# Optimization experiments

Measured on AMD Instinct MI355X. Metric: run time of the kernel, lower is better.

The kernel has to match this reference:

```python
import jax, jax.numpy as jnp
import numpy as np

# dims: B nodes, K hops, N neighbors/node, channels/features per FeatTrans1d stage
B, K, N = 512, 2, 32
C0, F0 = 1, 512
C1, F1 = 4, 16
C2, F2 = 32, 1
NUM_CLASS = 40
EPS_BN = 1e-5
EPS_NORM = 1e-7


def softsign(x):
    return x / (1.0 + jnp.abs(x))


def sgnroot(x):
    return jnp.sign(x) * jnp.sqrt(jnp.abs(x))


def row_normalize(x):
    # normalize over axis 1 as in the torch code; NaN -> 0
    x = x / (jnp.abs(x).sum(axis=1, keepdims=True) + EPS_NORM)
    return jnp.where(jnp.isnan(x), 0.0, x)


def feature_adjacency(x, nb):
    # x: [B,C,F], nb: [B,N,C,F] -> fadj: [B,F,F]
    fadj = jnp.einsum('bcf,bncg->bfg', x, nb)
    fadj = fadj + jnp.swapaxes(fadj, -1, -2)
    return row_normalize(sgnroot(fadj))


def transform(x, fadj, W):
    # x: [B,C,F], fadj: [B,F,G], W: [D,C,G,E] -> [B,D,E]
    xg = jnp.einsum('bcf,bfg->bcg', x, fadj)
    return jnp.einsum('bcg,dcge->bde', xg, W)


def transform_nb(nb, fadj, W):
    # nb: [B,N,C,F], fadj: [B,F,G] (node i's fadj broadcast over its N neighbors)
    xg = jnp.einsum('bncf,bfg->bncg', nb, fadj)
    return jnp.einsum('bncg,dcge->bnde', xg, W)


def bn(x, gamma, beta, axes, ch_axis):
    # training-mode BatchNorm1d: batch stats per channel (biased variance)
    mean = x.mean(axes, keepdims=True)
    var = x.var(axes, keepdims=True)
    shape = [1] * x.ndim
    shape[ch_axis] = x.shape[ch_axis]
    return (x - mean) * jax.lax.rsqrt(var + EPS_BN) * gamma.reshape(shape) + beta.reshape(shape)


def setup_inputs() -> dict:
    key = jax.random.key(0)
    ks = jax.random.split(key, 8)
    x = jax.random.normal(ks[0], (B, C0, F0), jnp.float32)
    neighbor = jax.random.normal(ks[1], (B, K, N, C0, F0), jnp.float32)
    W1 = jax.random.normal(ks[2], (K, C1, C0, F0, F1), jnp.float32) * 0.05
    W2 = jax.random.normal(ks[3], (K, C2, C1, F1, F2), jnp.float32) * 0.1
    g1 = jnp.ones((K, C1), jnp.float32)
    b1 = jnp.zeros((K, C1), jnp.float32)
    g2 = jnp.ones((K, C2), jnp.float32)
    b2 = jnp.zeros((K, C2), jnp.float32)
    Wc1 = jax.random.normal(ks[4], (C2 * F2 * K, C2 * F2), jnp.float32) * 0.1
    bc1 = jnp.zeros((C2 * F2,), jnp.float32)
    Wc2 = jax.random.normal(ks[5], (C2 * F2, NUM_CLASS), jnp.float32) * 0.1
    bc2 = jnp.zeros((NUM_CLASS,), jnp.float32)
    return {"x": x, "neighbor": neighbor, "W1": W1, "g1": g1, "b1": b1,
            "W2": W2, "g2": g2, "b2": b2,
            "Wc1": Wc1, "bc1": bc1, "Wc2": Wc2, "bc2": bc2}


def reference(x, neighbor, W1, g1, b1, W2, g2, b2, Wc1, bc1, Wc2, bc2):
    outs = []
    for kk in range(K):  # fixed small hop count, structurally distinct weights
        nb_k = neighbor[:, kk]                      # [B,N,C0,F0]
        fadj1 = feature_adjacency(x, nb_k)          # [B,F0,F0]
        h = transform(x, fadj1, W1[kk])             # [B,C1,F1]
        nbh = transform_nb(nb_k, fadj1, W1[kk])     # [B,N,C1,F1]
        # BN over batch+feature dims for h; per-node BN over (N,F) for neighbors
        h = softsign(bn(h, g1[kk], b1[kk], (0, 2), 1))
        nbh = softsign(bn(nbh, g1[kk], b1[kk], (1, 3), 2))
        fadj2 = feature_adjacency(h, nbh)           # [B,F1,F1]
        h2 = transform(h, fadj2, W2[kk])            # [B,C2,F2]
        h2 = softsign(bn(h2, g2[kk], b2[kk], (0, 2), 1))
        outs.append(h2)
    x_khops = jnp.concatenate(outs, axis=1)         # [B, C2*K, F2]
    flat = x_khops.reshape(B, -1)                   # dropout is identity at eval
    hid = jax.nn.relu(flat @ Wc1 + bc1)
    return hid @ Wc2 + bc2                          # [B, NUM_CLASS]
```

## Files before the change

kernel.cpp:

```cpp
#include <hip/hip_runtime.h>
#include <hip/hip_bf16.h>

#define B_SZ 512
#define KHOP 2
#define NNB  32
#define F0   512
#define C1   4
#define F1   16
#define C2   32
#define NCLS 40

#define EPS_BN   1e-5f
#define EPS_NORM 1e-7f

typedef __attribute__((ext_vector_type(8))) short short8;
typedef __attribute__((ext_vector_type(4))) float f32x4;

__device__ __forceinline__ float softsignf(float v) { return v / (1.0f + fabsf(v)); }

__device__ __forceinline__ unsigned cvt_pk_bf16(float lo, float hi) {
    unsigned r;
    asm("v_cvt_pk_bf16_f32 %0, %1, %2" : "=v"(r) : "v"(lo), "v"(hi));
    return r;
}

__global__ __launch_bounds__(256) void k_prep(const float* __restrict__ W1,
                                              unsigned short* __restrict__ w1t)
{
    const int idx = blockIdx.x * 256 + threadIdx.x;
    const int g  = idx & 511;
    const int de = (idx >> 9) & 63;
    const int kk = idx >> 15;
    const int d = de >> 4, e = de & 15;
    w1t[idx] = (unsigned short)cvt_pk_bf16(W1[((size_t)((kk * 4 + d) * 512) + g) * 16 + e], 0.f);
}

#define SMEM_MAIN 69632

__global__ __launch_bounds__(512, 4) void k_main(
    const float* __restrict__ xg_, const float* __restrict__ nbg,
    const unsigned short* __restrict__ w1t,
    const float* __restrict__ g1, const float* __restrict__ b1,
    float* __restrict__ h_raw, float* __restrict__ nbs_out,
    float* __restrict__ hsum)
{
    extern __shared__ char smem[];
    float* xl = (float*)(smem + 65536);
    float* sl = (float*)(smem + 67584);

    const int t = threadIdx.x;
    const int pair = blockIdx.x;
    const int b = pair >> 1, k = pair & 1;
    const int l = t & 63, w = t >> 6;
    const int m = w & 1, gsb = w >> 1;
    const int kol = l >> 4;
    const float* nbp = nbg + (size_t)pair * (NNB * F0);

    {
        const int oct = t & 63, ng = t >> 6;
        const int f0s = oct * 8;
        float sp0=0,sp1=0,sp2=0,sp3=0,sp4=0,sp5=0,sp6=0,sp7=0;
        #pragma unroll
        for (int ni = 0; ni < 4; ++ni) {
            const int n = ng * 4 + ni;
            float4 q0 = *(const float4*)(nbp + n * F0 + f0s);
            float4 q1 = *(const float4*)(nbp + n * F0 + f0s + 4);
            sp0 += q0.x; sp1 += q0.y; sp2 += q0.z; sp3 += q0.w;
            sp4 += q1.x; sp5 += q1.y; sp6 += q1.z; sp7 += q1.w;
            uint4 p;
            p.x = cvt_pk_bf16(q0.x, q0.y);
            p.y = cvt_pk_bf16(q0.z, q0.w);
            p.z = cvt_pk_bf16(q1.x, q1.y);
            p.w = cvt_pk_bf16(q1.z, q1.w);
            *(uint4*)(smem + n * 1024 + ((2 * f0s) ^ ((n & 7) << 4))) = p;
        }
        float* part = (float*)(smem + 32768);
        *(float4*)(part + ng * 512 + f0s)     = make_float4(sp0, sp1, sp2, sp3);
        *(float4*)(part + ng * 512 + f0s + 4) = make_float4(sp4, sp5, sp6, sp7);
        xl[t] = xg_[b * F0 + t];
    }
    __syncthreads();
    {
        const float* part = (const float*)(smem + 32768);
        float s = 0.f;
        #pragma unroll
        for (int p = 0; p < 8; ++p) s += part[p * 512 + t];
        sl[t] = s;
    }
    __syncthreads();

    const float xv = xl[t], sv = sl[t];
    float dS0 = 0.f, dS1 = 0.f, xS0 = 0.f, xS1 = 0.f;
    f32x4 acc[8];
    #pragma unroll
    for (int j = 0; j < 8; ++j) acc[j] = (f32x4){0.f, 0.f, 0.f, 0.f};

    const int swz = ((t >> 1) & 3) << 4;
    const int nA  = m * 16 + (l & 15);
    const int aSw = (nA & 7) << 4;

    #pragma unroll 1
    for (int strip = 0; strip < 16; ++strip) {
        const int f0 = strip * 32;
        #pragma unroll
        for (int ko = 0; ko < 4; ++ko) {
            float4 xf0 = ((const float4*)xl)[(f0 >> 2) + ko * 2];
            float4 xf1 = ((const float4*)xl)[(f0 >> 2) + ko * 2 + 1];
            float4 sf0 = ((const float4*)sl)[(f0 >> 2) + ko * 2];
            float4 sf1 = ((const float4*)sl)[(f0 >> 2) + ko * 2 + 1];
            const float xf[8] = {xf0.x, xf0.y, xf0.z, xf0.w, xf1.x, xf1.y, xf1.z, xf1.w};
            const float sf[8] = {sf0.x, sf0.y, sf0.z, sf0.w, sf1.x, sf1.y, sf1.z, sf1.w};
            unsigned pk[4];
            float vprev = 0.f;
            #pragma unroll
            for (int i = 0; i < 8; ++i) {
                float r = sf[i] * xv + xf[i] * sv;
                float a = sqrtf(fabsf(r));
                float v = copysignf(a, r);
                if (i & 1) {
                    dS1 += a; xS1 += xf[i] * v;
                    pk[i >> 1] = cvt_pk_bf16(vprev, v);
                } else {
                    dS0 += a; xS0 += xf[i] * v;
                    vprev = v;
                }
            }
            uint4 u; u.x = pk[0]; u.y = pk[1]; u.z = pk[2]; u.w = pk[3];
            *(uint4*)(smem + 32768 + t * 64 + ((ko * 16) ^ swz)) = u;
        }
        __syncthreads();
        short8 afrag = *(const short8*)(smem + nA * 1024 +
                        ((f0 * 2 + kol * 16) ^ aSw));
        #pragma unroll
        for (int j = 0; j < 8; ++j) {
            const int g = gsb * 128 + j * 16 + (l & 15);
            short8 bfrag = *(const short8*)(smem + 32768 + g * 64 +
                            ((kol * 16) ^ (((g >> 1) & 3) << 4)));
            acc[j] = __builtin_amdgcn_mfma_f32_16x16x32_bf16(afrag, bfrag, acc[j], 0, 0, 0);
        }
        __syncthreads();
    }

    {
        const float ia = 1.f / ((dS0 + dS1) + EPS_NORM);
        ((float*)(smem + 32768))[t] = ia;
        ((float*)(smem + 34816))[t] = (xS0 + xS1) * ia;
    }
    __syncthreads();

    {
        const float* invD = (const float*)(smem + 32768);
        #pragma unroll
        for (int j = 0; j < 8; ++j) {
            const int g = gsb * 128 + j * 16 + (l & 15);
            const float iv = invD[g];
            #pragma unroll
            for (int r = 0; r < 4; ++r) {
                const int n = m * 16 + (l >> 4) * 4 + r;
                *(unsigned short*)(smem + n * 1024 + ((2 * g) ^ ((n & 7) << 4))) =
                    (unsigned short)cvt_pk_bf16(acc[j][r] * iv, 0.f);
            }
        }
    }
    __syncthreads();

    f32x4 acc3 = (f32x4){0.f, 0.f, 0.f, 0.f};
    f32x4 acch = (f32x4){0.f, 0.f, 0.f, 0.f};
    {
        const int de = gsb * 16 + (l & 15);
        const unsigned short* wtp = w1t + ((size_t)(k * 64 + de) * 512) + kol * 8;
        const float* xgx = (const float*)(smem + 34816);
        #pragma unroll 2
        for (int ks = 0; ks < 16; ++ks) {
            short8 bfrag = *(const short8*)(wtp + ks * 32);
            short8 af = *(const short8*)(smem + nA * 1024 +
                        ((ks * 64 + kol * 16) ^ aSw));
            acc3 = __builtin_amdgcn_mfma_f32_16x16x32_bf16(af, bfrag, acc3, 0, 0, 0);
            if (m == 0) {
                short8 afh = {0, 0, 0, 0, 0, 0, 0, 0};
                if ((l & 15) == 0) {
                    float4 p0 = *(const float4*)(xgx + ks * 32 + kol * 8);
                    float4 p1 = *(const float4*)(xgx + ks * 32 + kol * 8 + 4);
                    uint4 pk;
                    pk.x = cvt_pk_bf16(p0.x, p0.y); pk.y = cvt_pk_bf16(p0.z, p0.w);
                    pk.z = cvt_pk_bf16(p1.x, p1.y); pk.w = cvt_pk_bf16(p1.z, p1.w);
                    __builtin_memcpy(&afh, &pk, 16);
                }
                acch = __builtin_amdgcn_mfma_f32_16x16x32_bf16(afh, bfrag, acch, 0, 0, 0);
            }
        }
    }

    float* redst = (float*)(smem + 32768);
    float* pnb   = (float*)(smem + 32832);
    {
        float vals[4];
        float s1 = 0.f, s2 = 0.f;
        #pragma unroll
        for (int r = 0; r < 4; ++r) {
            float v = acc3[r];
            vals[r] = v; s1 += v; s2 += v * v;
        }
        #pragma unroll
        for (int off = 32; off >= 1; off >>= 1) {
            s1 += __shfl_xor(s1, off);
            s2 += __shfl_xor(s2, off);
        }
        if (l == 0) { redst[w * 2] = s1; redst[w * 2 + 1] = s2; }
        __syncthreads();
        const float S1 = redst[w * 2]     + redst[(w ^ 1) * 2];
        const float S2 = redst[w * 2 + 1] + redst[(w ^ 1) * 2 + 1];
        const float mean = S1 * (1.f / 512.f);
        const float var  = S2 * (1.f / 512.f) - mean * mean;
        const float An   = g1[k * C1 + gsb] * rsqrtf(var + EPS_BN);
        const float Bn   = b1[k * C1 + gsb] - mean * An;
        float nbse = 0.f;
        #pragma unroll
        for (int r = 0; r < 4; ++r) nbse += softsignf(vals[r] * An + Bn);
        nbse += __shfl_xor(nbse, 16);
        nbse += __shfl_xor(nbse, 32);
        if (l < 16) pnb[m * 64 + gsb * 16 + l] = nbse;

        if (m == 0 && l < 16) {
            float hv = acch[0];
            h_raw[pair * 64 + gsb * 16 + l] = hv;
            float t1 = hv, t2 = hv * hv;
            #pragma unroll
            for (int off = 1; off <= 8; off <<= 1) {
                t1 += __shfl_xor(t1, off);
                t2 += __shfl_xor(t2, off);
            }
            if (l == 0) {
                atomicAdd(&hsum[k * 4 + gsb], t1);
                atomicAdd(&hsum[8 + k * 4 + gsb], t2);
            }
        }
    }
    __syncthreads();
    if (t < 64) nbs_out[pair * 64 + t] = pnb[t] + pnb[64 + t];
}

__global__ __launch_bounds__(256) void k_stage2(
    const float* __restrict__ h_rawg, const float* __restrict__ nbsg,
    const float* __restrict__ hsum,
    const float* __restrict__ g1, const float* __restrict__ b1,
    const float* __restrict__ W2,
    float* __restrict__ h2_raw, float* __restrict__ h2sum)
{
    __shared__ float hl[4][64], nl[4][64], fl[4][256], xg2l[4][64];
    const int t = threadIdx.x, wv = t >> 6, l = t & 63;
    const int pair = blockIdx.x * 4 + wv;
    const int k = pair & 1;
    const int d = l >> 4;
    {
        const float S1 = hsum[k * 4 + d], S2 = hsum[8 + k * 4 + d];
        const float mean = S1 * (1.f / 8192.f);
        const float var  = S2 * (1.f / 8192.f) - mean * mean;
        const float A = g1[k * 4 + d] * rsqrtf(var + EPS_BN);
        const float Bc = b1[k * 4 + d] - mean * A;
        float hv = h_rawg[pair * 64 + l];
        hl[wv][l] = softsignf(hv * A + Bc);
        nl[wv][l] = nbsg[pair * 64 + l];
    }
    __syncthreads();
    const int gcol = l & 15;
    float raw[4];
    #pragma unroll
    for (int j = 0; j < 4; ++j) {
        const int idx = l + 64 * j;
        const int f = idx >> 4;
        float a = 0.f;
        #pragma unroll
        for (int c = 0; c < 4; ++c) a += hl[wv][c * 16 + f] * nl[wv][c * 16 + gcol];
        raw[j] = a;
        fl[wv][idx] = a;
    }
    __syncthreads();
    float w4[4]; float Dp = 0.f;
    #pragma unroll
    for (int j = 0; j < 4; ++j) {
        const int idx = l + 64 * j;
        const int f = idx >> 4;
        float v = raw[j] + fl[wv][gcol * 16 + f];
        float a = sqrtf(fabsf(v));
        Dp += a;
        w4[j] = copysignf(a, v);
    }
    Dp += __shfl_xor(Dp, 16);
    Dp += __shfl_xor(Dp, 32);
    const float invD = 1.f / (Dp + EPS_NORM);
    __syncthreads();
    #pragma unroll
    for (int j = 0; j < 4; ++j) fl[wv][l + 64 * j] = w4[j] * invD;
    __syncthreads();
    {
        const int c = l >> 4;
        float a = 0.f;
        #pragma unroll
        for (int f = 0; f < 16; ++f) a += hl[wv][c * 16 + f] * fl[wv][f * 16 + gcol];
        xg2l[wv][c * 16 + gcol] = a;
    }
    __syncthreads();
    if (l < 32) {
        const float* W2p = W2 + k * (C2 * C1 * F1) + l * (C1 * F1);
        float a = 0.f;
        #pragma unroll
        for (int i = 0; i < 64; ++i) a += xg2l[wv][i] * W2p[i];
        h2_raw[pair * 32 + l] = a;
        atomicAdd(&h2sum[k * 32 + l], a);
        atomicAdd(&h2sum[64 + k * 32 + l], a * a);
    }
}

__global__ __launch_bounds__(64) void k_cls(
    const float* __restrict__ h2_raw, const float* __restrict__ h2sum,
    const float* __restrict__ g2, const float* __restrict__ b2,
    const float* __restrict__ Wc1, const float* __restrict__ bc1,
    const float* __restrict__ Wc2, const float* __restrict__ bc2,
    float* __restrict__ out)
{
    __shared__ float flat[64];
    __shared__ float hid[32];
    const int b = blockIdx.x, l = threadIdx.x;
    const int k = l >> 5, d = l & 31;
    {
        const float S1 = h2sum[l], S2 = h2sum[64 + l];
        const float mean = S1 * (1.f / 512.f);
        const float var  = S2 * (1.f / 512.f) - mean * mean;
        const float A = g2[l] * rsqrtf(var + EPS_BN);
        const float Bc = b2[l] - mean * A;
        float v = h2_raw[(b * 2 + k) * 32 + d];
        flat[l] = softsignf(v * A + Bc);
    }
    __syncthreads();
    if (l < 32) {
        float a = bc1[l];
        #pragma unroll
        for (int i = 0; i < 64; ++i) a += flat[i] * Wc1[i * 32 + l];
        hid[l] = fmaxf(a, 0.f);
    }
    __syncthreads();
    if (l < NCLS) {
        float a = bc2[l];
        #pragma unroll
        for (int j = 0; j < 32; ++j) a += hid[j] * Wc2[j * NCLS + l];
        out[b * NCLS + l] = a;
    }
}

extern "C" void kernel_launch(void* const* d_in, const int* in_sizes, int n_in,
                              void* d_out, int out_size, void* d_ws, size_t ws_size,
                              hipStream_t stream)
{
    const float* x   = (const float*)d_in[0];
    const float* nbg = (const float*)d_in[1];
    const float* W1  = (const float*)d_in[2];
    const float* g1  = (const float*)d_in[3];
    const float* b1  = (const float*)d_in[4];
    const float* W2  = (const float*)d_in[5];
    const float* g2  = (const float*)d_in[6];
    const float* b2  = (const float*)d_in[7];
    const float* Wc1 = (const float*)d_in[8];
    const float* bc1 = (const float*)d_in[9];
    const float* Wc2 = (const float*)d_in[10];
    const float* bc2 = (const float*)d_in[11];
    float* out = (float*)d_out;
    float* ws  = (float*)d_ws;

    float* h_raw  = ws;
    float* nbs    = ws + 65536;
    float* h2_raw = ws + 131072;
    float* stats  = ws + 163840;
    float* hsum   = stats;
    float* h2sum  = stats + 16;
    unsigned short* w1t = (unsigned short*)h2_raw;

    hipMemsetAsync(stats, 0, 144 * sizeof(float), stream);
    hipLaunchKernelGGL(k_prep,   dim3(256),             dim3(256), 0, stream, W1, w1t);
    hipLaunchKernelGGL(k_main,   dim3(B_SZ * KHOP),     dim3(512), SMEM_MAIN, stream,
                       x, nbg, w1t, g1, b1, h_raw, nbs, hsum);
    hipLaunchKernelGGL(k_stage2, dim3(B_SZ * KHOP / 4), dim3(256), 0, stream,
                       h_raw, nbs, hsum, g1, b1, W2, h2_raw, h2sum);
    hipLaunchKernelGGL(k_cls,    dim3(B_SZ),            dim3(64), 0, stream,
                       h2_raw, h2sum, g2, b2, Wc1, bc1, Wc2, bc2, out);
}
```

Measured before the change: 321.8 us.

## Double-buffer fadj strip tile, use raw v_sqrt, fold stats memset into prep

The main kernel's per-strip fadj tile in shared memory is now double-buffered by strip parity, which removes the trailing barrier in each strip iteration so one strip's compute can overlap the previous strip's MFMA reads. Shared memory grows from about 68KB to 100KB and the occupancy hint drops from 4 to 2 blocks per CU. The library sqrtf is replaced with the raw v_sqrt_f32 instruction, and the stats memset is folded into the prep kernel to save one launch.

New measurement: 301.8 us. 1.07x faster.

```diff
diff --git a/kernel.cpp b/kernel.cpp
--- a/kernel.cpp
+++ b/kernel.cpp
@@ -24,10 +24,18 @@
     return r;
 }
 
+__device__ __forceinline__ float vsqrtf(float x) {
+    float r;
+    asm("v_sqrt_f32 %0, %1" : "=v"(r) : "v"(x));
+    return r;
+}
+
 __global__ __launch_bounds__(256) void k_prep(const float* __restrict__ W1,
-                                              unsigned short* __restrict__ w1t)
+                                              unsigned short* __restrict__ w1t,
+                                              float* __restrict__ stats)
 {
     const int idx = blockIdx.x * 256 + threadIdx.x;
+    if (blockIdx.x == 0 && threadIdx.x < 144) stats[threadIdx.x] = 0.f;
     const int g  = idx & 511;
     const int de = (idx >> 9) & 63;
     const int kk = idx >> 15;
@@ -35,9 +43,10 @@
     w1t[idx] = (unsigned short)cvt_pk_bf16(W1[((size_t)((kk * 4 + d) * 512) + g) * 16 + e], 0.f);
 }
 
-#define SMEM_MAIN 69632
-
-__global__ __launch_bounds__(512, 4) void k_main(
+#define VT_BASE 32768
+#define SMEM_MAIN 102400
+
+__global__ __launch_bounds__(512, 2) void k_main(
     const float* __restrict__ xg_, const float* __restrict__ nbg,
     const unsigned short* __restrict__ w1t,
     const float* __restrict__ g1, const float* __restrict__ b1,
@@ -45,8 +54,8 @@
     float* __restrict__ hsum)
 {
     extern __shared__ char smem[];
-    float* xl = (float*)(smem + 65536);
-    float* sl = (float*)(smem + 67584);
+    float* xl = (float*)(smem + 98304);
+    float* sl = (float*)(smem + 100352);
 
     const int t = threadIdx.x;
     const int pair = blockIdx.x;
@@ -74,14 +83,14 @@
             p.w = cvt_pk_bf16(q1.z, q1.w);
             *(uint4*)(smem + n * 1024 + ((2 * f0s) ^ ((n & 7) << 4))) = p;
         }
-        float* part = (float*)(smem + 32768);
+        float* part = (float*)(smem + VT_BASE);
         *(float4*)(part + ng * 512 + f0s)     = make_float4(sp0, sp1, sp2, sp3);
         *(float4*)(part + ng * 512 + f0s + 4) = make_float4(sp4, sp5, sp6, sp7);
         xl[t] = xg_[b * F0 + t];
     }
     __syncthreads();
     {
-        const float* part = (const float*)(smem + 32768);
+        const float* part = (const float*)(smem + VT_BASE);
         float s = 0.f;
         #pragma unroll
         for (int p = 0; p < 8; ++p) s += part[p * 512 + t];
@@ -102,6 +111,7 @@
     #pragma unroll 1
     for (int strip = 0; strip < 16; ++strip) {
         const int f0 = strip * 32;
+        char* vt = smem + VT_BASE + ((strip & 1) << 15);
         #pragma unroll
         for (int ko = 0; ko < 4; ++ko) {
             float4 xf0 = ((const float4*)xl)[(f0 >> 2) + ko * 2];
@@ -115,7 +125,7 @@
             #pragma unroll
             for (int i = 0; i < 8; ++i) {
                 float r = sf[i] * xv + xf[i] * sv;
-                float a = sqrtf(fabsf(r));
+                float a = vsqrtf(fabsf(r));
                 float v = copysignf(a, r);
                 if (i & 1) {
                     dS1 += a; xS1 += xf[i] * v;
@@ -126,7 +136,7 @@
                 }
             }
             uint4 u; u.x = pk[0]; u.y = pk[1]; u.z = pk[2]; u.w = pk[3];
-            *(uint4*)(smem + 32768 + t * 64 + ((ko * 16) ^ swz)) = u;
+            *(uint4*)(vt + t * 64 + ((ko * 16) ^ swz)) = u;
         }
         __syncthreads();
         short8 afrag = *(const short8*)(smem + nA * 1024 +
@@ -134,22 +144,22 @@
         #pragma unroll
         for (int j = 0; j < 8; ++j) {
             const int g = gsb * 128 + j * 16 + (l & 15);
-            short8 bfrag = *(const short8*)(smem + 32768 + g * 64 +
+            short8 bfrag = *(const short8*)(vt + g * 64 +
                             ((kol * 16) ^ (((g >> 1) & 3) << 4)));
             acc[j] = __builtin_amdgcn_mfma_f32_16x16x32_bf16(afrag, bfrag, acc[j], 0, 0, 0);
         }
-        __syncthreads();
-    }
+    }
+    __syncthreads();
 
     {
         const float ia = 1.f / ((dS0 + dS1) + EPS_NORM);
-        ((float*)(smem + 32768))[t] = ia;
-        ((float*)(smem + 34816))[t] = (xS0 + xS1) * ia;
-    }
-    __syncthreads();
-
-    {
-        const float* invD = (const float*)(smem + 32768);
+        ((float*)(smem + VT_BASE))[t] = ia;
+        ((float*)(smem + VT_BASE + 2048))[t] = (xS0 + xS1) * ia;
+    }
+    __syncthreads();
+
+    {
+        const float* invD = (const float*)(smem + VT_BASE);
         #pragma unroll
         for (int j = 0; j < 8; ++j) {
             const int g = gsb * 128 + j * 16 + (l & 15);
@@ -169,7 +179,7 @@
     {
         const int de = gsb * 16 + (l & 15);
         const unsigned short* wtp = w1t + ((size_t)(k * 64 + de) * 512) + kol * 8;
-        const float* xgx = (const float*)(smem + 34816);
+        const float* xgx = (const float*)(smem + VT_BASE + 2048);
         #pragma unroll 2
         for (int ks = 0; ks < 16; ++ks) {
             short8 bfrag = *(const short8*)(wtp + ks * 32);
@@ -191,8 +201,8 @@
         }
     }
 
-    float* redst = (float*)(smem + 32768);
-    float* pnb   = (float*)(smem + 32832);
+    float* redst = (float*)(smem + 36864);
+    float* pnb   = (float*)(smem + 36928);
     {
         float vals[4];
         float s1 = 0.f, s2 = 0.f;
@@ -282,7 +292,7 @@
         const int idx = l + 64 * j;
         const int f = idx >> 4;
         float v = raw[j] + fl[wv][gcol * 16 + f];
-        float a = sqrtf(fabsf(v));
+        float a = vsqrtf(fabsf(v));
         Dp += a;
         w4[j] = copysignf(a, v);
     }
@@ -375,8 +385,7 @@
     float* h2sum  = stats + 16;
     unsigned short* w1t = (unsigned short*)h2_raw;
 
-    hipMemsetAsync(stats, 0, 144 * sizeof(float), stream);
-    hipLaunchKernelGGL(k_prep,   dim3(256),             dim3(256), 0, stream, W1, w1t);
+    hipLaunchKernelGGL(k_prep,   dim3(256),             dim3(256), 0, stream, W1, w1t, stats);
     hipLaunchKernelGGL(k_main,   dim3(B_SZ * KHOP),     dim3(512), SMEM_MAIN, stream,
                        x, nbg, w1t, g1, b1, h_raw, nbs, hsum);
     hipLaunchKernelGGL(k_stage2, dim3(B_SZ * KHOP / 4), dim3(256), 0, stream,
```
